# Optimization experiments

Hardware: AMD Instinct MI355X
Metric: run time of the kernel (lower is better)

The kernel has to match this reference:

```python
import jax, jax.numpy as jnp
import numpy as np

B = 16
COUNTS = np.array([6, 14, 10, 8, 16, 12, 9, 11, 7, 13, 10, 10, 8, 12, 6, 8], dtype=np.int64)  # sum=160, max=16
INPUT_DIM = 1024
D_IN = 834   # num_features_mixed4f + 2
G = 256      # num_features_gcn
NG = 4       # num_graphs
T, H, W = 8, 14, 14


def setup_inputs() -> dict:
    key = jax.random.key(0)
    ks = jax.random.split(key, 7)
    total = int(COUNTS.sum())
    return {
        "actor_features": jax.random.normal(ks[0], (total, INPUT_DIM), dtype=jnp.float32),
        "feature_map": jax.random.normal(ks[1], (B, D_IN, T, H, W), dtype=jnp.float32),
        "W_a": jax.random.normal(ks[2], (NG, G, INPUT_DIM), dtype=jnp.float32) * 0.02,
        "b_a": jnp.zeros((NG, G), dtype=jnp.float32),
        "W_c": jax.random.normal(ks[3], (NG, G, D_IN), dtype=jnp.float32) * 0.02,
        "b_c": jnp.zeros((NG, G), dtype=jnp.float32),
        "W_h": jax.random.normal(ks[4], (NG, G, G), dtype=jnp.float32) * 0.02,
        "num_actors_list": COUNTS,
        "return_features": 0,
    }


def _ragged_indices(counts):
    # static (concrete) ragged bookkeeping
    counts = np.asarray(counts)
    Bn = counts.shape[0]
    Nmax = int(counts.max())
    offsets = np.concatenate([np.zeros(1, np.int64), np.cumsum(counts)[:-1]])
    n = np.arange(Nmax)
    pad_idx = offsets[:, None] + np.minimum(n[None, :], counts[:, None] - 1)  # [B, Nmax]
    valid = (n[None, :] < counts[:, None])                                     # [B, Nmax]
    unpad_b = np.repeat(np.arange(Bn), counts)
    unpad_n = np.concatenate([np.arange(c) for c in counts])
    return pad_idx, valid, unpad_b, unpad_n


def reference(actor_features, feature_map, W_a, b_a, W_c, b_c, W_h,
              num_actors_list, return_features):
    pad_idx, valid, unpad_b, unpad_n = _ragged_indices(num_actors_list)
    valid_f = jnp.asarray(valid, actor_features.dtype)
    Bn = feature_map.shape[0]

    # actor embedding for all graphs: [total, ng, G]
    emb = jnp.einsum('td,gfd->tgf', actor_features, W_a) + b_a[None]
    # pad to [B, Nmax, ng, G]; zero padded slots (matches pad_sequence)
    padded = emb[pad_idx] * valid_f[:, :, None, None]

    # 1x1x1 conv == channel matmul over flattened spatio-temporal grid S=T*H*W
    fm = feature_map.reshape(Bn, feature_map.shape[1], -1)            # [B, C, S]
    ctx = jnp.einsum('bcs,gfc->bgfs', fm, W_c) + b_c[None, :, :, None]  # [B, ng, G, S]

    # adjacency: actor x context similarities, softmax over context locations
    adj = jnp.einsum('bngf,bgfs->bgns', padded, ctx)                  # [B, ng, Nmax, S]
    adj = jax.nn.softmax(adj, axis=-1)
    adj = adj * valid_f[:, None, :, None]                             # masked_fill pad rows -> 0

    # aggregate context + residual
    upd = jnp.einsum('bgns,bgfs->bngf', adj, ctx) + padded            # [B, Nmax, ng, G]

    # unpad back to ragged flat [total, ng, G] (dropout is identity in eval)
    flat = upd[unpad_b, unpad_n]
    out = jax.nn.relu(jnp.einsum('tgf,ghf->tgh', flat, W_h))          # head_linear + relu

    # func == 'concat': cat over graphs along feature dim -> [total, ng*G]
    return out.reshape(out.shape[0], -1)
```

## Files before the change

kernel.cpp:

```cpp
#include <hip/hip_runtime.h>

#define TOTAL   160
#define NMAX    16
#define INDIM   1024
#define DIN     834
#define KPAD    864
#define GF      256
#define SS      1568
#define SPAD    1664
#define CROW    264

__constant__ int c_counts[16] = {6,14,10,8,16,12,9,11,7,13,10,10,8,12,6,8};
__constant__ int c_offs[16]   = {0,6,20,30,38,54,66,75,86,93,106,116,126,134,146,152};
__constant__ int c_t0[8] = {0, 6, 12, 18, 25, 31, 37, 43};
__constant__ int c_t1[8] = {6, 12, 18, 25, 31, 37, 43, 49};

using bf16x8 = __attribute__((ext_vector_type(8))) short;
using f32x4  = __attribute__((ext_vector_type(4))) float;
using us4    = __attribute__((ext_vector_type(4))) unsigned short;

__device__ inline unsigned short f2bf(float f) {
  union { float f; unsigned u; } v; v.f = f;
  const unsigned u = v.u;
  return (unsigned short)((u + 0x7FFFu + ((u >> 16) & 1u)) >> 16);
}
__device__ inline float bf2f(unsigned short h) {
  union { unsigned u; float f; } v; v.u = ((unsigned)h) << 16; return v.f;
}

__device__ __forceinline__ void gload16(const unsigned short* g, unsigned short* l) {
  __builtin_amdgcn_global_load_lds(
      (const __attribute__((address_space(1))) unsigned int*)(g),
      (__attribute__((address_space(3))) unsigned int*)(l), 16, 0, 0);
}

__global__ __launch_bounds__(256) void prep_all(
    const float* __restrict__ actor, const float* __restrict__ Wa,
    const float* __restrict__ b_a, const float* __restrict__ Wc,
    const float* __restrict__ Wh, const float* __restrict__ fm,
    float* __restrict__ emb, unsigned short* __restrict__ emb_h,
    unsigned short* __restrict__ Ah, unsigned short* __restrict__ Wh_h,
    unsigned short* __restrict__ BhT)
{
  __shared__ float tile[32][33];
  __shared__ unsigned short As[64 * 40];
  __shared__ unsigned short Bs[64 * 40];
  const int bid = blockIdx.x, tid = threadIdx.x;

  if (bid < 48) {
    const int n0 = (bid & 15) * 64, m0 = (bid >> 4) * 64;
    const int wave = tid >> 6, lane = tid & 63;
    const int wm = (wave >> 1) * 32, wn = (wave & 1) * 32;
    const int quad = lane >> 4, lr = lane & 15;
    const int r = tid >> 2, ko = (tid & 3) * 8;
    const bool mval = (m0 + r < TOTAL);

    f32x4 acc[2][2];
    #pragma unroll
    for (int i = 0; i < 2; ++i)
      #pragma unroll
      for (int j = 0; j < 2; ++j) acc[i][j] = (f32x4){0.f, 0.f, 0.f, 0.f};

    const float4 zf4 = {0.f, 0.f, 0.f, 0.f};
    float4 ra0, ra1, rb0, rb1;
    ra0 = mval ? *reinterpret_cast<const float4*>(actor + (size_t)(m0 + r) * INDIM + ko) : zf4;
    ra1 = mval ? *reinterpret_cast<const float4*>(actor + (size_t)(m0 + r) * INDIM + ko + 4) : zf4;
    rb0 = *reinterpret_cast<const float4*>(Wa + (size_t)(n0 + r) * INDIM + ko);
    rb1 = *reinterpret_cast<const float4*>(Wa + (size_t)(n0 + r) * INDIM + ko + 4);

    for (int kt = 0; kt < 32; ++kt) {
      __syncthreads();
      {
        us4 a0, a1, b0, b1;
        a0[0]=f2bf(ra0.x); a0[1]=f2bf(ra0.y); a0[2]=f2bf(ra0.z); a0[3]=f2bf(ra0.w);
        a1[0]=f2bf(ra1.x); a1[1]=f2bf(ra1.y); a1[2]=f2bf(ra1.z); a1[3]=f2bf(ra1.w);
        b0[0]=f2bf(rb0.x); b0[1]=f2bf(rb0.y); b0[2]=f2bf(rb0.z); b0[3]=f2bf(rb0.w);
        b1[0]=f2bf(rb1.x); b1[1]=f2bf(rb1.y); b1[2]=f2bf(rb1.z); b1[3]=f2bf(rb1.w);
        *reinterpret_cast<us4*>(&As[r * 40 + ko])     = a0;
        *reinterpret_cast<us4*>(&As[r * 40 + ko + 4]) = a1;
        *reinterpret_cast<us4*>(&Bs[r * 40 + ko])     = b0;
        *reinterpret_cast<us4*>(&Bs[r * 40 + ko + 4]) = b1;
      }
      __syncthreads();
      if (kt < 31) {
        const int k0 = (kt + 1) * 32;
        ra0 = mval ? *reinterpret_cast<const float4*>(actor + (size_t)(m0 + r) * INDIM + k0 + ko) : zf4;
        ra1 = mval ? *reinterpret_cast<const float4*>(actor + (size_t)(m0 + r) * INDIM + k0 + ko + 4) : zf4;
        rb0 = *reinterpret_cast<const float4*>(Wa + (size_t)(n0 + r) * INDIM + k0 + ko);
        rb1 = *reinterpret_cast<const float4*>(Wa + (size_t)(n0 + r) * INDIM + k0 + ko + 4);
      }
      bf16x8 af[2], bfr[2];
      #pragma unroll
      for (int i = 0; i < 2; ++i)
        af[i] = *reinterpret_cast<const bf16x8*>(&As[(wm + i * 16 + lr) * 40 + quad * 8]);
      #pragma unroll
      for (int j = 0; j < 2; ++j)
        bfr[j] = *reinterpret_cast<const bf16x8*>(&Bs[(wn + j * 16 + lr) * 40 + quad * 8]);
      #pragma unroll
      for (int i = 0; i < 2; ++i)
        #pragma unroll
        for (int j = 0; j < 2; ++j)
          acc[i][j] = __builtin_amdgcn_mfma_f32_16x16x32_bf16(af[i], bfr[j], acc[i][j], 0, 0, 0);
    }

    #pragma unroll
    for (int i = 0; i < 2; ++i) {
      #pragma unroll
      for (int reg = 0; reg < 4; ++reg) {
        const int m = m0 + wm + i * 16 + quad * 4 + reg;
        if (m >= TOTAL) continue;
        #pragma unroll
        for (int j = 0; j < 2; ++j) {
          const int n = n0 + wn + j * 16 + lr;
          const float v = acc[i][j][reg] + b_a[n];
          emb[(size_t)m * INDIM + n] = v;
          emb_h[(size_t)m * INDIM + n] = f2bf(v);
        }
      }
    }
  } else if (bid < 3760) {
    const int pb = bid - 48;
    if (pb < 3456) {
      const int idx = pb * 256 + tid;
      const int k = idx % KPAD, gm = idx / KPAD;
      Ah[idx] = (k < DIN) ? f2bf(Wc[gm * DIN + k]) : (unsigned short)0;
    } else {
      const int i = (pb - 3456) * 256 + tid;
      const float4 v = reinterpret_cast<const float4*>(Wh)[i];
      us4 o; o[0] = f2bf(v.x); o[1] = f2bf(v.y); o[2] = f2bf(v.z); o[3] = f2bf(v.w);
      reinterpret_cast<us4*>(Wh_h)[i] = o;
    }
  } else {
    const int fb = bid - 3760;
    const int sx = fb % 49, ky = (fb / 49) % 27, b = fb / (49 * 27);
    const int k0 = ky * 32, s0 = sx * 32;
    const int tx = tid & 31, ty = tid >> 5;
    const float* src = fm + (size_t)b * DIN * SS;
    #pragma unroll
    for (int r = 0; r < 4; ++r) {
      const int k = k0 + ty + r * 8;
      tile[ty + r * 8][tx] = (k < DIN) ? src[(size_t)k * SS + s0 + tx] : 0.f;
    }
    __syncthreads();
    unsigned short* dst = BhT + (size_t)b * SS * KPAD;
    #pragma unroll
    for (int r = 0; r < 4; ++r) {
      const int s = s0 + ty + r * 8;
      dst[(size_t)s * KPAD + k0 + tx] = f2bf(tile[tx][ty + r * 8]);
    }
  }
}

__global__ __launch_bounds__(256, 3) void ctx_mfma(const unsigned short* __restrict__ Ah,
                                                   const unsigned short* __restrict__ BhT,
                                                   const float* __restrict__ b_c,
                                                   unsigned short* __restrict__ ctxT) {
  __shared__ unsigned short As[128 * 32];
  __shared__ unsigned short Bs[128 * 32];
  const int lin  = blockIdx.x;
  const int xcd  = lin & 7;
  const int slot = lin >> 3;
  const int bloc = (slot >= 104) ? 1 : 0;
  const int within = slot - bloc * 104;
  const int b  = xcd * 2 + bloc;
  const int mt = within % 13;
  const int gn = within / 13;
  const int g  = gn & 3;
  const int n0 = (gn >> 2) * 128;
  const int m0 = mt * 128;
  const int zout = (g << 4) + b;

  const int tid = threadIdx.x;
  const int wave = tid >> 6, lane = tid & 63;
  const int wm = (wave >> 1) * 64, wn = (wave & 1) * 64;
  const int quad = lane >> 4, lr = lane & 15;

  const unsigned short* Ag = BhT + (size_t)b * SS * KPAD + (size_t)m0 * KPAD;
  const unsigned short* Bg = Ah + (size_t)g * 256 * KPAD + (size_t)n0 * KPAD;

  const int srow  = wave * 16 + (lane >> 2);
  const int skoff = (lane & 3) * 8;
  unsigned short* ldsA0 = As + (wave * 16) * 32;
  unsigned short* ldsA1 = As + (64 + wave * 16) * 32;
  unsigned short* ldsB0 = Bs + (wave * 16) * 32;
  unsigned short* ldsB1 = Bs + (64 + wave * 16) * 32;

  f32x4 acc[4][4];
  #pragma unroll
  for (int i = 0; i < 4; ++i)
    #pragma unroll
    for (int j = 0; j < 4; ++j) acc[i][j] = (f32x4){0.f, 0.f, 0.f, 0.f};

  for (int kt = 0; kt < 27; ++kt) {
    const int k0 = kt * 32 + skoff;
    gload16(Ag + (size_t)srow * KPAD + k0,        ldsA0);
    gload16(Ag + (size_t)(srow + 64) * KPAD + k0, ldsA1);
    gload16(Bg + (size_t)srow * KPAD + k0,        ldsB0);
    gload16(Bg + (size_t)(srow + 64) * KPAD + k0, ldsB1);
    __syncthreads();

    bf16x8 af[4], bfr[4];
    #pragma unroll
    for (int i = 0; i < 4; ++i)
      af[i] = *reinterpret_cast<const bf16x8*>(&As[(wm + i * 16 + lr) * 32 + quad * 8]);
    #pragma unroll
    for (int j = 0; j < 4; ++j)
      bfr[j] = *reinterpret_cast<const bf16x8*>(&Bs[(wn + j * 16 + lr) * 32 + quad * 8]);
    #pragma unroll
    for (int i = 0; i < 4; ++i)
      #pragma unroll
      for (int j = 0; j < 4; ++j)
        acc[i][j] = __builtin_amdgcn_mfma_f32_16x16x32_bf16(af[i], bfr[j], acc[i][j], 0, 0, 0);
    __syncthreads();
  }

  unsigned short* Cz = ctxT + (size_t)zout * SPAD * GF;
  const float* bias = b_c + g * GF;
  #pragma unroll
  for (int j = 0; j < 4; ++j) {
    const int n = n0 + wn + j * 16 + lr;
    const float bv = bias[n];
    #pragma unroll
    for (int i = 0; i < 4; ++i) {
      #pragma unroll
      for (int reg = 0; reg < 4; ++reg) {
        const int m = m0 + wm + i * 16 + quad * 4 + reg;
        Cz[(size_t)m * GF + n] = f2bf(acc[i][j][reg] + bv);
      }
    }
  }
}

__global__ __launch_bounds__(256) void att_part(
    const unsigned short* __restrict__ ctxT,
    const unsigned short* __restrict__ emb_h,
    float* __restrict__ Opart,
    float* __restrict__ Spart)
{
  __shared__ unsigned short Cs[4][32 * CROW];
  __shared__ float Ps[4][32][20];
  __shared__ float walpha[4][16];
  __shared__ float wms[4][16], wls[4][16];
  const int sc = blockIdx.x, z = blockIdx.y;
  const int g = z >> 4, b = z & 15;
  const int count = c_counts[b], off = c_offs[b];
  const int t0 = c_t0[sc], t1 = c_t1[sc];
  const int tid = threadIdx.x, wave = tid >> 6, lane = tid & 63;
  const int quad = lane >> 4, lr = lane & 15;
  const unsigned short* Az = ctxT + (size_t)z * SPAD * GF;
  const bool bvalid = (lr < count);
  const unsigned short* Brow = emb_h + (size_t)(off + (bvalid ? lr : 0)) * INDIM + (g << 8);
  unsigned short* myC = &Cs[wave][0];
  const int fbase = quad * 64 + lr * 4;
  const bf16x8 zero8 = (bf16x8)(short)0;

  float O[16][4];
  #pragma unroll
  for (int n = 0; n < 16; ++n)
    #pragma unroll
    for (int j = 0; j < 4; ++j) O[n][j] = 0.f;
  float m_run = -3.0e38f, l_run = 0.f;

  for (int t = t0 + wave; t < t1; t += 4) {
    const int s0 = t * 32;
    #pragma unroll
    for (int q = 0; q < 16; ++q) {
      const int row = 2 * q + (lane >> 5);
      const int col = (lane & 31) * 8;
      const uint4 v = *reinterpret_cast<const uint4*>(Az + (size_t)(s0 + row) * GF + col);
      *reinterpret_cast<uint4*>(&myC[row * CROW + col]) = v;
    }
    f32x4 acc[2] = {(f32x4){0.f,0.f,0.f,0.f}, (f32x4){0.f,0.f,0.f,0.f}};
    #pragma unroll
    for (int kk = 0; kk < 8; ++kk) {
      const int f = kk * 32 + quad * 8;
      bf16x8 bv8 = *reinterpret_cast<const bf16x8*>(Brow + f);
      if (!bvalid) bv8 = zero8;
      #pragma unroll
      for (int i = 0; i < 2; ++i) {
        const bf16x8 av8 = *reinterpret_cast<const bf16x8*>(&myC[(i * 16 + lr) * CROW + f]);
        acc[i] = __builtin_amdgcn_mfma_f32_16x16x32_bf16(av8, bv8, acc[i], 0, 0, 0);
      }
    }
    float mx = acc[0][0];
    #pragma unroll
    for (int i = 0; i < 2; ++i)
      #pragma unroll
      for (int r = 0; r < 4; ++r) mx = fmaxf(mx, acc[i][r]);
    float lsum = 0.f;
    #pragma unroll
    for (int i = 0; i < 2; ++i)
      #pragma unroll
      for (int r = 0; r < 4; ++r) lsum += __expf(acc[i][r] - mx);
    #pragma unroll
    for (int d = 16; d < 64; d <<= 1) {
      const float om = __shfl_xor(mx, d, 64);
      const float ol = __shfl_xor(lsum, d, 64);
      const float M = fmaxf(mx, om);
      lsum = lsum * __expf(mx - M) + ol * __expf(om - M);
      mx = M;
    }
    const float m_new = fmaxf(m_run, mx);
    const float alpha = __expf(m_run - m_new);
    const float beta  = __expf(mx - m_new);
    l_run = alpha * l_run + beta * lsum;
    m_run = m_new;
    if (lane < 16) walpha[wave][lane] = alpha;
    #pragma unroll
    for (int i = 0; i < 2; ++i)
      #pragma unroll
      for (int r = 0; r < 4; ++r) {
        const int sl = i * 16 + quad * 4 + r;
        Ps[wave][sl][lr] = beta * __expf(acc[i][r] - mx);
      }
    float av[16];
    {
      const float4 a0 = *reinterpret_cast<const float4*>(&walpha[wave][0]);
      const float4 a1 = *reinterpret_cast<const float4*>(&walpha[wave][4]);
      const float4 a2 = *reinterpret_cast<const float4*>(&walpha[wave][8]);
      const float4 a3 = *reinterpret_cast<const float4*>(&walpha[wave][12]);
      av[0]=a0.x; av[1]=a0.y; av[2]=a0.z; av[3]=a0.w;
      av[4]=a1.x; av[5]=a1.y; av[6]=a1.z; av[7]=a1.w;
      av[8]=a2.x; av[9]=a2.y; av[10]=a2.z; av[11]=a2.w;
      av[12]=a3.x; av[13]=a3.y; av[14]=a3.z; av[15]=a3.w;
    }
    #pragma unroll
    for (int n = 0; n < 16; ++n)
      #pragma unroll
      for (int j = 0; j < 4; ++j) O[n][j] *= av[n];
    for (int s = 0; s < 32; ++s) {
      const float4 p0 = *reinterpret_cast<const float4*>(&Ps[wave][s][0]);
      const float4 p1 = *reinterpret_cast<const float4*>(&Ps[wave][s][4]);
      const float4 p2 = *reinterpret_cast<const float4*>(&Ps[wave][s][8]);
      const float4 p3 = *reinterpret_cast<const float4*>(&Ps[wave][s][12]);
      const us4 cv = *reinterpret_cast<const us4*>(&myC[s * CROW + fbase]);
      const float c0 = bf2f(cv[0]), c1 = bf2f(cv[1]), c2 = bf2f(cv[2]), c3 = bf2f(cv[3]);
      const float pn[16] = {p0.x,p0.y,p0.z,p0.w, p1.x,p1.y,p1.z,p1.w,
                            p2.x,p2.y,p2.z,p2.w, p3.x,p3.y,p3.z,p3.w};
      #pragma unroll
      for (int n = 0; n < 16; ++n) {
        O[n][0] = fmaf(pn[n], c0, O[n][0]);
        O[n][1] = fmaf(pn[n], c1, O[n][1]);
        O[n][2] = fmaf(pn[n], c2, O[n][2]);
        O[n][3] = fmaf(pn[n], c3, O[n][3]);
      }
    }
  }

  if (lane < 16) { wms[wave][lane] = m_run; wls[wave][lane] = l_run; }
  __syncthreads();
  float* Ob = reinterpret_cast<float*>(&Cs[wave][0]);
  #pragma unroll
  for (int n = 0; n < 16; ++n) {
    const float Mb = fmaxf(fmaxf(wms[0][n], wms[1][n]), fmaxf(wms[2][n], wms[3][n]));
    const float e = __expf(wms[wave][n] - Mb);
    #pragma unroll
    for (int j = 0; j < 4; ++j) Ob[n * 256 + fbase + j] = O[n][j] * e;
  }
  __syncthreads();
  float* Op = Opart + ((size_t)z * 8 + sc) * 4096;
  #pragma unroll
  for (int nn = 0; nn < 4; ++nn) {
    const int n = wave * 4 + nn;
    float4 v = {0.f, 0.f, 0.f, 0.f};
    #pragma unroll
    for (int w = 0; w < 4; ++w) {
      const float4 x = *reinterpret_cast<const float4*>(
          reinterpret_cast<const float*>(&Cs[w][0]) + n * 256 + fbase);
      v.x += x.x; v.y += x.y; v.z += x.z; v.w += x.w;
    }
    *reinterpret_cast<float4*>(Op + n * 256 + fbase) = v;
  }
  if (wave == 0 && lane < 16) {
    const int n = lane;
    const float Mb = fmaxf(fmaxf(wms[0][n], wms[1][n]), fmaxf(wms[2][n], wms[3][n]));
    float Lb = 0.f;
    #pragma unroll
    for (int w = 0; w < 4; ++w) Lb += wls[w][n] * __expf(wms[w][n] - Mb);
    Spart[((size_t)z * 8 + sc) * 32 + n]      = Mb;
    Spart[((size_t)z * 8 + sc) * 32 + 16 + n] = Lb;
  }
}

__global__ __launch_bounds__(256) void att_combine(
    const float* __restrict__ Opart, const float* __restrict__ Spart,
    const float* __restrict__ emb, unsigned short* __restrict__ flat_h) {
  const int z = blockIdx.x, n = blockIdx.y;
  const int g = z >> 4, b = z & 15;
  const int count = c_counts[b], off = c_offs[b];
  if (n >= count) return;
  const int f = threadIdx.x;
  float M = -3.0e38f;
  #pragma unroll
  for (int sc = 0; sc < 8; ++sc)
    M = fmaxf(M, Spart[((size_t)z * 8 + sc) * 32 + n]);
  float L = 0.f, acc = 0.f;
  #pragma unroll
  for (int sc = 0; sc < 8; ++sc) {
    const float e = __expf(Spart[((size_t)z * 8 + sc) * 32 + n] - M);
    L += e * Spart[((size_t)z * 8 + sc) * 32 + 16 + n];
    acc += e * Opart[((size_t)z * 8 + sc) * 4096 + n * 256 + f];
  }
  const int t = off + n;
  const int col = (g << 8) + f;
  flat_h[t * INDIM + col] = f2bf(acc / L + emb[t * INDIM + col]);
}

__global__ __launch_bounds__(256) void head_mfma(const unsigned short* __restrict__ flat_h,
                                                 const unsigned short* __restrict__ Wh_h,
                                                 float* __restrict__ out) {
  __shared__ unsigned short As[64 * 40];
  __shared__ unsigned short Bs[64 * 40];
  const int g = blockIdx.z;
  const int n0 = blockIdx.x * 64, m0 = blockIdx.y * 64;
  const int tid = threadIdx.x;
  const int wave = tid >> 6, lane = tid & 63;
  const int wm = (wave >> 1) * 32, wn = (wave & 1) * 32;
  const int quad = lane >> 4, lr = lane & 15;
  const int r = tid >> 2, ko = (tid & 3) * 8;

  const unsigned short* Ag = flat_h + (size_t)m0 * INDIM + g * GF;
  const unsigned short* Bg = Wh_h + (size_t)g * GF * GF + (size_t)n0 * GF;

  f32x4 acc[2][2];
  #pragma unroll
  for (int i = 0; i < 2; ++i)
    #pragma unroll
    for (int j = 0; j < 2; ++j) acc[i][j] = (f32x4){0.f, 0.f, 0.f, 0.f};

  const uint4 zero4 = {0u, 0u, 0u, 0u};
  uint4 ra, rb;
  ra = (m0 + r < TOTAL) ? *reinterpret_cast<const uint4*>(Ag + (size_t)r * INDIM + ko) : zero4;
  rb = *reinterpret_cast<const uint4*>(Bg + (size_t)r * GF + ko);

  for (int kt = 0; kt < 8; ++kt) {
    __syncthreads();
    *reinterpret_cast<uint4*>(&As[r * 40 + ko]) = ra;
    *reinterpret_cast<uint4*>(&Bs[r * 40 + ko]) = rb;
    __syncthreads();
    if (kt < 7) {
      const int k0 = (kt + 1) * 32;
      ra = (m0 + r < TOTAL) ? *reinterpret_cast<const uint4*>(Ag + (size_t)r * INDIM + k0 + ko) : zero4;
      rb = *reinterpret_cast<const uint4*>(Bg + (size_t)r * GF + k0 + ko);
    }
    bf16x8 af[2], bfr[2];
    #pragma unroll
    for (int i = 0; i < 2; ++i)
      af[i] = *reinterpret_cast<const bf16x8*>(&As[(wm + i * 16 + lr) * 40 + quad * 8]);
    #pragma unroll
    for (int j = 0; j < 2; ++j)
      bfr[j] = *reinterpret_cast<const bf16x8*>(&Bs[(wn + j * 16 + lr) * 40 + quad * 8]);
    #pragma unroll
    for (int i = 0; i < 2; ++i)
      #pragma unroll
      for (int j = 0; j < 2; ++j)
        acc[i][j] = __builtin_amdgcn_mfma_f32_16x16x32_bf16(af[i], bfr[j], acc[i][j], 0, 0, 0);
  }

  #pragma unroll
  for (int i = 0; i < 2; ++i) {
    #pragma unroll
    for (int reg = 0; reg < 4; ++reg) {
      const int m = m0 + wm + i * 16 + quad * 4 + reg;
      if (m >= TOTAL) continue;
      #pragma unroll
      for (int j = 0; j < 2; ++j) {
        const int n = n0 + wn + j * 16 + lr;
        out[(size_t)m * INDIM + g * GF + n] = fmaxf(acc[i][j][reg], 0.f);
      }
    }
  }
}

extern "C" void kernel_launch(void* const* d_in, const int* in_sizes, int n_in,
                              void* d_out, int out_size, void* d_ws, size_t ws_size,
                              hipStream_t stream) {
  (void)in_sizes; (void)n_in; (void)out_size; (void)ws_size;
  const float* actor = (const float*)d_in[0];
  const float* fmap  = (const float*)d_in[1];
  const float* W_a   = (const float*)d_in[2];
  const float* b_a   = (const float*)d_in[3];
  const float* W_c   = (const float*)d_in[4];
  const float* b_c   = (const float*)d_in[5];
  const float* W_h   = (const float*)d_in[6];
  float* out = (float*)d_out;
  char* ws = (char*)d_ws;

  float* emb             = (float*)(ws);
  unsigned short* flat_h = (unsigned short*)(ws + 655360);
  unsigned short* emb_h  = (unsigned short*)(ws + 983040);
  float* Spart           = (float*)(ws + 1310720);
  unsigned short* ctxT   = (unsigned short*)(ws + 1376256);
  unsigned short* Ah     = (unsigned short*)(ws + 55902208);
  unsigned short* BhT    = (unsigned short*)(ws + 57671680);
  float* Opart           = (float*)(ws + 57671680);
  unsigned short* Wh_h   = (unsigned short*)(ws + 101023744);

  hipLaunchKernelGGL(prep_all, dim3(24928), dim3(256), 0, stream,
                     actor, W_a, b_a, W_c, W_h, fmap,
                     emb, emb_h, Ah, Wh_h, BhT);

  hipLaunchKernelGGL(ctx_mfma, dim3(1664), dim3(256), 0, stream, Ah, BhT, b_c, ctxT);

  hipLaunchKernelGGL(att_part, dim3(8, 64), dim3(256), 0, stream,
                     ctxT, emb_h, Opart, Spart);

  hipLaunchKernelGGL(att_combine, dim3(64, 16), dim3(256), 0, stream,
                     Opart, Spart, emb, flat_h);

  hipLaunchKernelGGL(head_mfma, dim3(4, 3, 4), dim3(256), 0, stream,
                     flat_h, Wh_h, out);
}
```

Measured before the change: 265.4 us.

## Enlarge ctx GEMM tiles to 256x256 with 4-stage async LDS pipeline and swizzle

The context 1x1x1-conv GEMM now uses 512-thread blocks, each computing a 256x256 output tile (the full feature dimension per graph) instead of 128x128, which cuts the grid from 1664 to 448 blocks and raises data reuse per load. K-tiles are loaded into a 4-deep ring buffer in LDS using direct-to-LDS loads issued three stages ahead, with explicit vmcnt waits and a single barrier per step, so memory traffic overlaps the MFMA work. LDS addresses are XOR-swizzled to avoid bank conflicts, and output rows past the padded length are guarded. The cost is heavier register use (8x4 accumulators per wave) and lower occupancy, plus more work in the partially empty last M tile.

```diff
diff --git a/kernel.cpp b/kernel.cpp
--- a/kernel.cpp
+++ b/kernel.cpp
@@ -151,81 +151,119 @@
   }
 }
 
-__global__ __launch_bounds__(256, 3) void ctx_mfma(const unsigned short* __restrict__ Ah,
+__global__ __launch_bounds__(512, 2) void ctx_mfma(const unsigned short* __restrict__ Ah,
                                                    const unsigned short* __restrict__ BhT,
                                                    const float* __restrict__ b_c,
                                                    unsigned short* __restrict__ ctxT) {
-  __shared__ unsigned short As[128 * 32];
-  __shared__ unsigned short Bs[128 * 32];
+  __shared__ unsigned short ABuf[4][2][8192];
   const int lin  = blockIdx.x;
   const int xcd  = lin & 7;
   const int slot = lin >> 3;
-  const int bloc = (slot >= 104) ? 1 : 0;
-  const int within = slot - bloc * 104;
+  const int bloc = (slot >= 28) ? 1 : 0;
+  const int within = slot - bloc * 28;
   const int b  = xcd * 2 + bloc;
-  const int mt = within % 13;
-  const int gn = within / 13;
-  const int g  = gn & 3;
-  const int n0 = (gn >> 2) * 128;
-  const int m0 = mt * 128;
+  const int mt = within % 7;
+  const int g  = within / 7;
+  const int m0 = mt * 256;
   const int zout = (g << 4) + b;
 
   const int tid = threadIdx.x;
-  const int wave = tid >> 6, lane = tid & 63;
-  const int wm = (wave >> 1) * 64, wn = (wave & 1) * 64;
+  const int w    = tid >> 6, lane = tid & 63;
+  const int wm   = (w >> 2) * 128;
+  const int wn   = (w & 3) * 64;
   const int quad = lane >> 4, lr = lane & 15;
 
   const unsigned short* Ag = BhT + (size_t)b * SS * KPAD + (size_t)m0 * KPAD;
-  const unsigned short* Bg = Ah + (size_t)g * 256 * KPAD + (size_t)n0 * KPAD;
-
-  const int srow  = wave * 16 + (lane >> 2);
-  const int skoff = (lane & 3) * 8;
-  unsigned short* ldsA0 = As + (wave * 16) * 32;
-  unsigned short* ldsA1 = As + (64 + wave * 16) * 32;
-  unsigned short* ldsB0 = Bs + (wave * 16) * 32;
-  unsigned short* ldsB1 = Bs + (64 + wave * 16) * 32;
-
-  f32x4 acc[4][4];
-  #pragma unroll
-  for (int i = 0; i < 4; ++i)
+  const unsigned short* Bg = Ah + (size_t)g * 256 * KPAD;
+
+  int rS[2], kS[2];
+  #pragma unroll
+  for (int p = 0; p < 2; ++p) {
+    const int o    = p * 8192 + w * 1024 + lane * 16;
+    const int line = o >> 7;
+    const int gs   = (o >> 4) & 7;
+    const int gg   = gs ^ (line & 7);
+    rS[p] = line * 2 + (gg >> 2);
+    kS[p] = (gg & 3) * 8;
+  }
+
+  int offA[8], offB[4];
+  #pragma unroll
+  for (int i = 0; i < 8; ++i) {
+    const int r = wm + i * 16 + lr;
+    const int line = r >> 1;
+    const int gs = ((r & 1) * 4 + quad) ^ (line & 7);
+    offA[i] = line * 64 + gs * 8;
+  }
+  #pragma unroll
+  for (int j = 0; j < 4; ++j) {
+    const int r = wn + j * 16 + lr;
+    const int line = r >> 1;
+    const int gs = ((r & 1) * 4 + quad) ^ (line & 7);
+    offB[j] = line * 64 + gs * 8;
+  }
+
+  f32x4 acc[8][4];
+  #pragma unroll
+  for (int i = 0; i < 8; ++i)
     #pragma unroll
     for (int j = 0; j < 4; ++j) acc[i][j] = (f32x4){0.f, 0.f, 0.f, 0.f};
 
-  for (int kt = 0; kt < 27; ++kt) {
-    const int k0 = kt * 32 + skoff;
-    gload16(Ag + (size_t)srow * KPAD + k0,        ldsA0);
-    gload16(Ag + (size_t)(srow + 64) * KPAD + k0, ldsA1);
-    gload16(Bg + (size_t)srow * KPAD + k0,        ldsB0);
-    gload16(Bg + (size_t)(srow + 64) * KPAD + k0, ldsB1);
-    __syncthreads();
-
-    bf16x8 af[4], bfr[4];
-    #pragma unroll
-    for (int i = 0; i < 4; ++i)
-      af[i] = *reinterpret_cast<const bf16x8*>(&As[(wm + i * 16 + lr) * 32 + quad * 8]);
-    #pragma unroll
-    for (int j = 0; j < 4; ++j)
-      bfr[j] = *reinterpret_cast<const bf16x8*>(&Bs[(wn + j * 16 + lr) * 32 + quad * 8]);
-    #pragma unroll
-    for (int i = 0; i < 4; ++i)
-      #pragma unroll
-      for (int j = 0; j < 4; ++j)
-        acc[i][j] = __builtin_amdgcn_mfma_f32_16x16x32_bf16(af[i], bfr[j], acc[i][j], 0, 0, 0);
-    __syncthreads();
-  }
+#define CTX_ISSUE(KT) {                                                              \
+    const int bsel_ = (KT) & 3;                                                      \
+    _Pragma("unroll")                                                                \
+    for (int p = 0; p < 2; ++p) {                                                    \
+      gload16(Ag + (size_t)rS[p] * KPAD + (KT) * 32 + kS[p],                         \
+              &ABuf[bsel_][0][p * 4096 + w * 512]);                                  \
+      gload16(Bg + (size_t)rS[p] * KPAD + (KT) * 32 + kS[p],                         \
+              &ABuf[bsel_][1][p * 4096 + w * 512]);                                  \
+    } }
+
+#define CTX_BODY(KT, WAITSTR, DOISSUE) {                                             \
+    asm volatile(WAITSTR ::: "memory");                                              \
+    __builtin_amdgcn_s_barrier();                                                    \
+    if (DOISSUE) CTX_ISSUE((KT) + 3);                                                \
+    const unsigned short* Ab_ = &ABuf[(KT) & 3][0][0];                               \
+    const unsigned short* Bb_ = &ABuf[(KT) & 3][1][0];                               \
+    bf16x8 af[8], bv[4];                                                             \
+    _Pragma("unroll")                                                                \
+    for (int j = 0; j < 4; ++j) bv[j] = *reinterpret_cast<const bf16x8*>(&Bb_[offB[j]]); \
+    _Pragma("unroll")                                                                \
+    for (int i = 0; i < 8; ++i) af[i] = *reinterpret_cast<const bf16x8*>(&Ab_[offA[i]]); \
+    _Pragma("unroll")                                                                \
+    for (int i = 0; i < 8; ++i)                                                      \
+      _Pragma("unroll")                                                              \
+      for (int j = 0; j < 4; ++j)                                                    \
+        acc[i][j] = __builtin_amdgcn_mfma_f32_16x16x32_bf16(af[i], bv[j], acc[i][j], 0, 0, 0); \
+  }
+
+  CTX_ISSUE(0);
+  CTX_ISSUE(1);
+  CTX_ISSUE(2);
+
+  #pragma unroll 4
+  for (int kt = 0; kt < 24; ++kt) {
+    CTX_BODY(kt, "s_waitcnt vmcnt(8)", 1);
+  }
+  CTX_BODY(24, "s_waitcnt vmcnt(8)", 0);
+  CTX_BODY(25, "s_waitcnt vmcnt(4)", 0);
+  CTX_BODY(26, "s_waitcnt vmcnt(0)", 0);
+
+#undef CTX_BODY
+#undef CTX_ISSUE
 
   unsigned short* Cz = ctxT + (size_t)zout * SPAD * GF;
   const float* bias = b_c + g * GF;
   #pragma unroll
   for (int j = 0; j < 4; ++j) {
-    const int n = n0 + wn + j * 16 + lr;
+    const int n = wn + j * 16 + lr;
     const float bv = bias[n];
     #pragma unroll
-    for (int i = 0; i < 4; ++i) {
+    for (int i = 0; i < 8; ++i) {
       #pragma unroll
       for (int reg = 0; reg < 4; ++reg) {
         const int m = m0 + wm + i * 16 + quad * 4 + reg;
-        Cz[(size_t)m * GF + n] = f2bf(acc[i][j][reg] + bv);
+        if (m < SPAD) Cz[(size_t)m * GF + n] = f2bf(acc[i][j][reg] + bv);
       }
     }
   }
@@ -500,7 +538,7 @@
                      actor, W_a, b_a, W_c, W_h, fmap,
                      emb, emb_h, Ah, Wh_h, BhT);
 
-  hipLaunchKernelGGL(ctx_mfma, dim3(1664), dim3(256), 0, stream, Ah, BhT, b_c, ctxT);
+  hipLaunchKernelGGL(ctx_mfma, dim3(448), dim3(512), 0, stream, Ah, BhT, b_c, ctxT);
 
   hipLaunchKernelGGL(att_part, dim3(8, 64), dim3(256), 0, stream,
                      ctxT, emb_h, Opart, Spart);
```

After: 294.5 us. 11.0% more time.

## Triple-buffer ctx GEMM LDS tiles with swizzled layout and async prefetch

Applied to the files above, without the earlier changes.

Restructures the ctx_mfma K loop into a 3-stage LDS ring. Global-to-LDS loads for tile kt+3 are issued while MFMAs run on tile kt, gated by explicit vmcnt waits and raw barriers. LDS rows are XOR-swizzled to avoid bank conflicts on the bf16x8 fragment reads. LDS use rises to 48KB per block, which may limit the 3-blocks-per-CU occupancy, and the hand-written waitcnt counts must match the number of loads in flight.

```diff
diff --git a/kernel.cpp b/kernel.cpp
--- a/kernel.cpp
+++ b/kernel.cpp
@@ -155,8 +155,7 @@
                                                    const unsigned short* __restrict__ BhT,
                                                    const float* __restrict__ b_c,
                                                    unsigned short* __restrict__ ctxT) {
-  __shared__ unsigned short As[128 * 32];
-  __shared__ unsigned short Bs[128 * 32];
+  __shared__ unsigned short ABuf[3][2][4096];
   const int lin  = blockIdx.x;
   const int xcd  = lin & 7;
   const int slot = lin >> 3;
@@ -171,19 +170,39 @@
   const int zout = (g << 4) + b;
 
   const int tid = threadIdx.x;
-  const int wave = tid >> 6, lane = tid & 63;
-  const int wm = (wave >> 1) * 64, wn = (wave & 1) * 64;
+  const int w = tid >> 6, lane = tid & 63;
+  const int wm = (w >> 1) * 64, wn = (w & 1) * 64;
   const int quad = lane >> 4, lr = lane & 15;
 
   const unsigned short* Ag = BhT + (size_t)b * SS * KPAD + (size_t)m0 * KPAD;
   const unsigned short* Bg = Ah + (size_t)g * 256 * KPAD + (size_t)n0 * KPAD;
 
-  const int srow  = wave * 16 + (lane >> 2);
-  const int skoff = (lane & 3) * 8;
-  unsigned short* ldsA0 = As + (wave * 16) * 32;
-  unsigned short* ldsA1 = As + (64 + wave * 16) * 32;
-  unsigned short* ldsB0 = Bs + (wave * 16) * 32;
-  unsigned short* ldsB1 = Bs + (64 + wave * 16) * 32;
+  int rS[2], kS[2];
+  #pragma unroll
+  for (int p = 0; p < 2; ++p) {
+    const int o    = p * 4096 + w * 1024 + lane * 16;
+    const int line = o >> 7;
+    const int gs   = (o >> 4) & 7;
+    const int gg   = gs ^ (line & 7);
+    rS[p] = line * 2 + (gg >> 2);
+    kS[p] = (gg & 3) * 8;
+  }
+
+  int offA[4], offB[4];
+  #pragma unroll
+  for (int i = 0; i < 4; ++i) {
+    const int r = wm + i * 16 + lr;
+    const int line = r >> 1;
+    const int gs = ((r & 1) * 4 + quad) ^ (line & 7);
+    offA[i] = line * 64 + gs * 8;
+  }
+  #pragma unroll
+  for (int j = 0; j < 4; ++j) {
+    const int r = wn + j * 16 + lr;
+    const int line = r >> 1;
+    const int gs = ((r & 1) * 4 + quad) ^ (line & 7);
+    offB[j] = line * 64 + gs * 8;
+  }
 
   f32x4 acc[4][4];
   #pragma unroll
@@ -191,41 +210,65 @@
     #pragma unroll
     for (int j = 0; j < 4; ++j) acc[i][j] = (f32x4){0.f, 0.f, 0.f, 0.f};
 
-  for (int kt = 0; kt < 27; ++kt) {
-    const int k0 = kt * 32 + skoff;
-    gload16(Ag + (size_t)srow * KPAD + k0,        ldsA0);
-    gload16(Ag + (size_t)(srow + 64) * KPAD + k0, ldsA1);
-    gload16(Bg + (size_t)srow * KPAD + k0,        ldsB0);
-    gload16(Bg + (size_t)(srow + 64) * KPAD + k0, ldsB1);
-    __syncthreads();
-
-    bf16x8 af[4], bfr[4];
-    #pragma unroll
-    for (int i = 0; i < 4; ++i)
-      af[i] = *reinterpret_cast<const bf16x8*>(&As[(wm + i * 16 + lr) * 32 + quad * 8]);
-    #pragma unroll
-    for (int j = 0; j < 4; ++j)
-      bfr[j] = *reinterpret_cast<const bf16x8*>(&Bs[(wn + j * 16 + lr) * 32 + quad * 8]);
-    #pragma unroll
-    for (int i = 0; i < 4; ++i)
-      #pragma unroll
-      for (int j = 0; j < 4; ++j)
-        acc[i][j] = __builtin_amdgcn_mfma_f32_16x16x32_bf16(af[i], bfr[j], acc[i][j], 0, 0, 0);
-    __syncthreads();
-  }
+#define CTX_ISSUE(KT, BUF) {                                                          \
+    _Pragma("unroll")                                                                 \
+    for (int p = 0; p < 2; ++p) {                                                     \
+      gload16(Ag + (size_t)rS[p] * KPAD + (KT) * 32 + kS[p],                          \
+              &ABuf[BUF][0][p * 2048 + w * 512]);                                     \
+      gload16(Bg + (size_t)rS[p] * KPAD + (KT) * 32 + kS[p],                          \
+              &ABuf[BUF][1][p * 2048 + w * 512]);                                     \
+    } }
+
+#define CTX_BODY(KT, BUF, WAITSTR, DOISSUE) {                                         \
+    asm volatile(WAITSTR ::: "memory");                                               \
+    __builtin_amdgcn_s_barrier();                \
+    bf16x8 af[4], bv[4];                                                              \
+    _Pragma("unroll")                                                                 \
+    for (int j = 0; j < 4; ++j)                                                       \
+      bv[j] = *reinterpret_cast<const bf16x8*>(&ABuf[BUF][1][offB[j]]);               \
+    _Pragma("unroll")                                                                 \
+    for (int i = 0; i < 4; ++i)                                                       \
+      af[i] = *reinterpret_cast<const bf16x8*>(&ABuf[BUF][0][offA[i]]);               \
+    asm volatile("s_waitcnt lgkmcnt(0)" ::: "memory");                                \
+    __builtin_amdgcn_sched_barrier(0);                                                \
+    __builtin_amdgcn_s_barrier();                      \
+    if (DOISSUE) CTX_ISSUE((KT) + 3, BUF);              \
+    _Pragma("unroll")                                                                 \
+    for (int i = 0; i < 4; ++i)                                                       \
+      _Pragma("unroll")                                                               \
+      for (int j = 0; j < 4; ++j)                                                     \
+        acc[i][j] = __builtin_amdgcn_mfma_f32_16x16x32_bf16(af[i], bv[j], acc[i][j], 0, 0, 0); \
+  }
+
+  CTX_ISSUE(0, 0);
+  CTX_ISSUE(1, 1);
+  CTX_ISSUE(2, 2);
+
+  for (int kt = 0; kt < 24; kt += 3) {
+    CTX_BODY(kt,     0, "s_waitcnt vmcnt(8)", 1);
+    CTX_BODY(kt + 1, 1, "s_waitcnt vmcnt(8)", 1);
+    CTX_BODY(kt + 2, 2, "s_waitcnt vmcnt(8)", 1);
+  }
+  CTX_BODY(24, 0, "s_waitcnt vmcnt(8)", 0);
+  CTX_BODY(25, 1, "s_waitcnt vmcnt(4)", 0);
+  CTX_BODY(26, 2, "s_waitcnt vmcnt(0)", 0);
+
+#undef CTX_BODY
+#undef CTX_ISSUE
 
   unsigned short* Cz = ctxT + (size_t)zout * SPAD * GF;
   const float* bias = b_c + g * GF;
-  #pragma unroll
-  for (int j = 0; j < 4; ++j) {
-    const int n = n0 + wn + j * 16 + lr;
-    const float bv = bias[n];
-    #pragma unroll
-    for (int i = 0; i < 4; ++i) {
-      #pragma unroll
-      for (int reg = 0; reg < 4; ++reg) {
-        const int m = m0 + wm + i * 16 + quad * 4 + reg;
-        Cz[(size_t)m * GF + n] = f2bf(acc[i][j][reg] + bv);
+  float bvj[4];
+  #pragma unroll
+  for (int j = 0; j < 4; ++j) bvj[j] = bias[n0 + wn + j * 16 + lr];
+  #pragma unroll
+  for (int i = 0; i < 4; ++i) {
+    #pragma unroll
+    for (int reg = 0; reg < 4; ++reg) {
+      const int m = m0 + wm + i * 16 + quad * 4 + reg;
+      #pragma unroll
+      for (int j = 0; j < 4; ++j) {
+        Cz[(size_t)m * GF + n0 + wn + j * 16 + lr] = f2bf(acc[i][j][reg] + bvj[j]);
       }
     }
   }
```

After: 268.4 us. About the same (+1.1%).
